# Kernel optimization log

Measured on AMD Instinct MI355X. Metric: run time of the kernel, lower is better.

Reference implementation:

```python
import jax, jax.numpy as jnp
import numpy as np
from jax import lax

B, PH, PW, D = 4, 256, 256, 128
WS, SS, NG, NH = 8, 4, 2, 4
HID = int(D * 2.0)
DC = D // 2  # ngram-context channel dim


def _window_partition(x, ws):
    b, h, w, c = x.shape
    x = x.reshape(b, h // ws, ws, w // ws, ws, c).transpose(0, 1, 3, 2, 4, 5)
    return x.reshape(-1, ws, ws, c), (h // ws, w // ws)


def _window_unpartition(win, nwin):
    wh, ww = nwin
    _, s1, s2, c = win.shape
    x = win.reshape(-1, wh, ww, s1, s2, c).transpose(0, 1, 3, 2, 4, 5)
    return x.reshape(-1, wh * s1, ww * s2, c)


def _rel_pos_index(wh, ww):
    coords = np.stack(np.meshgrid(np.arange(wh), np.arange(ww), indexing='ij')).reshape(2, -1)
    rel = (coords[:, :, None] - coords[:, None, :]).transpose(1, 2, 0)
    rel[:, :, 0] += wh - 1
    rel[:, :, 1] += ww - 1
    rel[:, :, 0] *= 2 * ww - 1
    return rel.sum(-1)  # [N, N]

RPI_MAIN = jnp.asarray(_rel_pos_index(WS, WS))
RPI_NG = jnp.asarray(_rel_pos_index(NG, NG))


def _layernorm(x, g, b, eps=1e-5):
    mu = x.mean(-1, keepdims=True)
    var = ((x - mu) ** 2).mean(-1, keepdims=True)
    return (x - mu) * lax.rsqrt(var + eps) * g + b


def _mhsa(x, qkv_w, qkv_b, proj_w, proj_b, bias_table, rpi, nheads, mask=None):
    b_, n, c = x.shape
    hd = c // nheads
    qkv = (x @ qkv_w.T + qkv_b).reshape(b_, n, 3, nheads, hd).transpose(2, 0, 3, 1, 4)
    q, k, v = qkv[0] * (hd ** -0.5), qkv[1], qkv[2]
    attn = jnp.einsum('bhnd,bhmd->bhnm', q, k) + bias_table[rpi].transpose(2, 0, 1)[None]
    if mask is not None:
        nw = mask.shape[0]
        attn = (attn.reshape(b_ // nw, nw, nheads, n, n) + mask[None, :, None]).reshape(b_, nheads, n, n)
    attn = jax.nn.softmax(attn, axis=-1)
    out = jnp.einsum('bhnm,bhmd->bhnd', attn, v).transpose(0, 2, 1, 3).reshape(b_, n, c)
    return out @ proj_w.T + proj_b


def _make_mask(ph, pw):
    img = np.zeros((ph, pw), np.float32)
    cnt = 0
    for h in (slice(0, -WS), slice(-WS, -SS), slice(-SS, None)):
        for w in (slice(0, -WS), slice(-WS, -SS), slice(-SS, None)):
            img[h, w] = cnt
            cnt += 1
    mw, _ = _window_partition(jnp.asarray(img)[None, :, :, None], WS)
    mw = mw.reshape(-1, WS * WS)
    diff = mw[:, None, :] - mw[:, :, None]
    return jnp.where(diff != 0, -100.0, 0.0)  # [wh*ww, WS*WS, WS*WS]


def _seq_refl_pad(u, back):
    # sequential reflective window pad by ngram-1 on H and W (front if back else end)
    nh, nw = u.shape[2], u.shape[3]
    if back:
        ih = np.concatenate([np.arange(1, NG), np.arange(nh)])
        iw = np.concatenate([np.arange(1, NG), np.arange(nw)])
    else:
        ih = np.concatenate([np.arange(nh), np.arange(nh - NG, nh - 1)])
        iw = np.concatenate([np.arange(nw), np.arange(nw - NG, nw - 1)])
    return u[:, :, ih][:, :, :, iw]


def _sliding_attn(u, ng_qkv_w, ng_qkv_b, ng_proj_w, ng_proj_b, ng_bias, wh, ww):
    # u: [B, DC, wh+NG-1, ww+NG-1]  (padded unigram)
    hi = (np.arange(wh)[:, None] + np.arange(NG)[None, :]).reshape(-1)
    wi = (np.arange(ww)[:, None] + np.arange(NG)[None, :]).reshape(-1)
    slide = u[:, :, hi][:, :, :, wi].transpose(0, 2, 3, 1)  # [B, wh*NG, ww*NG, DC]
    win, nwin = _window_partition(slide, NG)
    win = win.reshape(-1, NG * NG, DC)
    ctx = _mhsa(win, ng_qkv_w, ng_qkv_b, ng_proj_w, ng_proj_b, ng_bias, RPI_NG, NH)
    ctx = _window_unpartition(ctx.reshape(-1, NG, NG, DC), nwin)  # [B, wh*NG, ww*NG, DC]
    ctx = ctx.transpose(0, 3, 1, 2)
    b = ctx.shape[0]
    return ctx.reshape(b, DC, wh, NG, ww, NG).mean(axis=(3, 5))  # AvgPool2d(NG) -> [B, DC, wh, ww]


def reference(x, uni_w, uni_b, ng_qkv_w, ng_qkv_b, ng_proj_w, ng_proj_b, ng_bias,
              merge_w, merge_b, qkv_w, qkv_b, proj_w, proj_b, bias_table,
              n1_g, n1_b, n2_g, n2_b, fc1_w, fc1_b, fc2_w, fc2_b, ph, pw):
    b = x.shape[0]
    xi = x.reshape(b, ph, pw, D)
    wh, ww = ph // WS, pw // WS
    # --- NGram context ---
    xc = xi.transpose(0, 3, 1, 2)  # NCHW
    uni = lax.conv_general_dilated(xc, uni_w, (WS, WS), 'VALID', feature_group_count=DC,
                                   dimension_numbers=('NCHW', 'OIHW', 'NCHW'))
    uni = uni + uni_b[None, :, None, None]  # [B, DC, wh, ww]
    ctx_f = _sliding_attn(_seq_refl_pad(uni, False), ng_qkv_w, ng_qkv_b, ng_proj_w, ng_proj_b, ng_bias, wh, ww)
    ctx_b = _sliding_attn(_seq_refl_pad(uni, True), ng_qkv_w, ng_qkv_b, ng_proj_w, ng_proj_b, ng_bias, wh, ww)
    ctx = jnp.concatenate([ctx_f, ctx_b], axis=1)  # [B, D, wh, ww]
    ctx = jnp.einsum('bchw,oc->bohw', ctx, merge_w) + merge_b[None, :, None, None]  # 1x1 merge conv
    ctx = ctx.transpose(0, 2, 3, 1)  # [B, wh, ww, D]
    # --- inject context into semi-partitioned windows ---
    windows = xi.reshape(b, wh, WS, ww, WS, D).transpose(0, 1, 3, 2, 4, 5)  # [B, wh, ww, WS, WS, D]
    windows = windows + ctx[:, :, :, None, None, :]
    xw = windows.transpose(0, 1, 3, 2, 4, 5).reshape(b, ph, pw, D)
    # --- cyclic shift + masked window attention ---
    xw = jnp.roll(xw, (-SS, -SS), axis=(1, 2))
    win, _ = _window_partition(xw, WS)
    win = win.reshape(-1, WS * WS, D)
    mask = _make_mask(ph, pw)
    aw = _mhsa(win, qkv_w, qkv_b, proj_w, proj_b, bias_table, RPI_MAIN, NH, mask=mask)
    shifted = _window_unpartition(aw.reshape(-1, WS, WS, D), (wh, ww))  # [B, ph, pw, D]
    rev = jnp.roll(shifted, (SS, SS), axis=(1, 2)).reshape(b, ph * pw, D)
    # --- residual + post-branch layernorm, then FFN ---
    x1 = x + _layernorm(rev, n1_g, n1_b)
    h = jax.nn.gelu(x1 @ fc1_w.T + fc1_b, approximate=False)
    ffn = h @ fc2_w.T + fc2_b
    return x1 + _layernorm(ffn, n2_g, n2_b)


def setup_inputs() -> dict:
    key = jax.random.key(0)
    ks = jax.random.split(key, 12)
    w = lambda k, shape: jax.random.normal(k, shape, jnp.float32) * 0.02
    return {
        'x': jax.random.normal(ks[0], (B, PH * PW, D), jnp.float32),
        'uni_w': w(ks[1], (DC, 2, WS, WS)),
        'uni_b': jnp.zeros((DC,), jnp.float32),
        'ng_qkv_w': w(ks[2], (3 * DC, DC)),
        'ng_qkv_b': jnp.zeros((3 * DC,), jnp.float32),
        'ng_proj_w': w(ks[3], (DC, DC)),
        'ng_proj_b': jnp.zeros((DC,), jnp.float32),
        'ng_bias': w(ks[4], ((2 * NG - 1) ** 2, NH)),
        'merge_w': w(ks[5], (D, D)),
        'merge_b': jnp.zeros((D,), jnp.float32),
        'qkv_w': w(ks[6], (3 * D, D)),
        'qkv_b': jnp.zeros((3 * D,), jnp.float32),
        'proj_w': w(ks[7], (D, D)),
        'proj_b': jnp.zeros((D,), jnp.float32),
        'bias_table': w(ks[8], ((2 * WS - 1) ** 2, NH)),
        'n1_g': jnp.ones((D,), jnp.float32),
        'n1_b': jnp.zeros((D,), jnp.float32),
        'n2_g': jnp.ones((D,), jnp.float32),
        'n2_b': jnp.zeros((D,), jnp.float32),
        'fc1_w': w(ks[9], (HID, D)),
        'fc1_b': jnp.zeros((HID,), jnp.float32),
        'fc2_w': w(ks[10], (D, HID)),
        'fc2_b': jnp.zeros((D,), jnp.float32),
        'ph': PH,
        'pw': PW,
    }
```

## Files before the change

kernel.cpp:

```cpp
#include <hip/hip_runtime.h>

typedef __bf16 bf16x8 __attribute__((ext_vector_type(8)));
typedef float  f32x4  __attribute__((ext_vector_type(4)));

#define QSCALE 0.17677669529663687f
#define XF_LD 130

__device__ __forceinline__ f32x4 mfma16(bf16x8 a, bf16x8 b, f32x4 c) {
  return __builtin_amdgcn_mfma_f32_16x16x32_bf16(a, b, c, 0, 0, 0);
}

__device__ __forceinline__ int swz_idx(int row, int col, int rowChunks) {
  return row * (rowChunks << 3) + ((((col >> 3) ^ (row & 7)) << 3) | (col & 7));
}

__device__ __forceinline__ bf16x8 ld_tile(const __bf16* t, int rowChunks,
                                          int rowBase, int chunkBase, int lane) {
  int row = rowBase + (lane & 15);
  int c = (chunkBase + (lane >> 4)) ^ (row & 7);
  return *(const bf16x8*)(t + row * (rowChunks << 3) + (c << 3));
}

__device__ __forceinline__ bf16x8 ld_pack(const __bf16* pk, int nt, int ks,
                                          int ksteps, int lane) {
  int idx = ((nt * ksteps + ks) * 64 + lane) * 8;
  return *(const bf16x8*)(pk + idx);
}

__global__ void k_prep(const float* __restrict__ qkvw, const float* __restrict__ projw,
                       const float* __restrict__ fc1w, const float* __restrict__ fc2w,
                       const float* __restrict__ ngprojw, const float* __restrict__ ngprojb,
                       const float* __restrict__ mergew, const float* __restrict__ mergeb,
                       const float* __restrict__ bt,
                       const float* __restrict__ x, const float* __restrict__ uw,
                       const float* __restrict__ ub,
                       __bf16* __restrict__ pk, float* __restrict__ w12T,
                       float* __restrict__ fb, float* __restrict__ btf,
                       float* __restrict__ uni) {
  int blk = blockIdx.x;
  if (blk < 2048) {
    int bidx = blk * 2 + (threadIdx.x >> 7);
    int b = bidx >> 10, oh = (bidx >> 5) & 31, ow = bidx & 31;
    int d = threadIdx.x & 127;
    const float* xb = x + (((size_t)((b << 16) + ((oh << 3) << 8) + (ow << 3))) << 7) + d;
    const float* w = uw + d * 64;
    float acc = 0.f;
#pragma unroll
    for (int kh = 0; kh < 8; ++kh)
#pragma unroll
      for (int kw = 0; kw < 8; ++kw)
        acc += xb[(size_t)(((kh << 8) + kw)) << 7] * w[kh * 8 + kw];
    acc += __shfl_xor(acc, 1);
    if (!(d & 1)) uni[((size_t)bidx << 6) + (d >> 1)] = acc + ub[d >> 1];
  } else if (blk < 2560) {
    int i = (blk - 2048) * 256 + threadIdx.x;
    const float* src; int K; int e; int scaleQ = 0;
    if (i < 32768)      { src = qkvw;             K = 128; e = i;          scaleQ = 1; }
    else if (i < 49152) { src = qkvw + 256 * 128; K = 128; e = i - 32768; }
    else if (i < 65536) { src = projw;            K = 128; e = i - 49152; }
    else if (i < 98304) { src = fc1w;             K = 128; e = i - 65536; }
    else                { src = fc2w;             K = 256; e = i - 98304; }
    int i8 = e & 7, ln = (e >> 3) & 63, t = e >> 9;
    int ls = (K == 256) ? 3 : 2;
    int ks = t & ((1 << ls) - 1), nt = t >> ls;
    int row = (nt << 4) + (ln & 15);
    int k = (ks << 5) + ((ln >> 4) << 3) + i8;
    float v = src[row * K + k];
    if (scaleQ && row < 128) v *= QSCALE;
    pk[i] = (__bf16)v;
  } else if (blk < 2816) {
    int idx = (blk - 2560) * 256 + threadIdx.x;
    int v = idx >> 14, h = (idx >> 12) & 3, n = (idx >> 6) & 63, m = idx & 63;
    int s1n = n >> 3, s2n = n & 7, s1m = m >> 3, s2m = m & 7;
    int rpi = (s1n - s1m + 7) * 15 + (s2n - s2m + 7);
    float val = bt[rpi * 4 + h];
    if (((v & 1) && ((s1n < 4) != (s1m < 4))) ||
        ((v & 2) && ((s2n < 4) != (s2m < 4))))
      val -= 100.f;
    btf[idx] = val;
  } else {
    int idx = (blk - 2816) * 256 + threadIdx.x;
    if (idx < 16384) {
      int which = idx >> 13;
      int r = idx & 8191;
      int e = r >> 7, o = r & 127;
      float a = 0.f;
#pragma unroll 8
      for (int d = 0; d < 64; ++d)
        a += mergew[o * 128 + which * 64 + d] * ngprojw[d * 64 + e];
      w12T[idx] = a;
    } else if (idx < 16384 + 128) {
      int o = idx - 16384;
      float a = mergeb[o];
#pragma unroll 8
      for (int d = 0; d < 64; ++d)
        a += (mergew[o * 128 + d] + mergew[o * 128 + 64 + d]) * ngprojb[d];
      fb[o] = a;
    }
  }
}

__global__ void __launch_bounds__(256, 1)
k_ngram(const float* __restrict__ uni, const float* __restrict__ ngqkvw,
        const float* __restrict__ ngqkvb, const float* __restrict__ ngbias,
        const float* __restrict__ w12T, const float* __restrict__ fbg,
        float* __restrict__ ctx) {
  extern __shared__ float sm[];
  float* qkvT = sm;
  float* w1T  = qkvT + 12288;
  float* w2T  = w1T + 8192;
  float* tokl = w2T + 8192;
  float* qs   = tokl + 2304;
  float* prs  = qs + 6912;
  float* avgl = prs + 256;
  float* ngb  = avgl + 1024;
  float* fbs  = ngb + 192;
  float* nbias= fbs + 128;

  const int t = threadIdx.x;
  const int bidx = blockIdx.x;
  const int b = bidx >> 7, ii = (bidx >> 2) & 31, jq = bidx & 3;
  const int j0 = jq * 8;

#pragma unroll
  for (int it = 0; it < 12; ++it) {
    int f = it * 256 + t;
    int o = f >> 4, c4 = (f & 15) << 2;
    float4 v = *(const float4*)(ngqkvw + o * 64 + c4);
    float s = (o < 64) ? 0.25f : 1.f;
    qkvT[(c4 + 0) * 192 + o] = v.x * s;
    qkvT[(c4 + 1) * 192 + o] = v.y * s;
    qkvT[(c4 + 2) * 192 + o] = v.z * s;
    qkvT[(c4 + 3) * 192 + o] = v.w * s;
  }
#pragma unroll
  for (int it = 0; it < 16; ++it) {
    int f = (it * 256 + t) << 2;
    *(float4*)(w1T + f) = *(const float4*)(w12T + f);
  }
  if (t < 192) ngb[t] = ngqkvb[t] * (t < 64 ? 0.25f : 1.f);
  if (t < 128) fbs[t] = fbg[t];
  if (t < 36)  nbias[t] = ngbias[t];
  {
    int w = t >> 6, lane = t & 63;
    int dir = w >> 1, rr = w & 1;
    int pi = ii + rr;
    int srcr = (dir == 0) ? ((pi < 32) ? pi : 30) : ((pi == 0) ? 1 : pi - 1);
#pragma unroll
    for (int cc = 0; cc < 9; ++cc) {
      int pj = j0 + cc;
      int srcc = (dir == 0) ? ((pj < 32) ? pj : 30) : ((pj == 0) ? 1 : pj - 1);
      tokl[((dir * 2 + rr) * 9 + cc) * 64 + lane] =
          uni[(size_t)((b * 32 + srcr) * 32 + srcc) * 64 + lane];
    }
  }
  __syncthreads();

  {
    int w = t >> 6, lane = t & 63;
    for (int itp = 0; itp < 9; ++itp) {
      int pos = itp * 4 + w;
      const float* tk = tokl + pos * 64;
      float a0 = ngb[lane], a1 = ngb[64 + lane], a2 = ngb[128 + lane];
#pragma unroll 4
      for (int c = 0; c < 64; ++c) {
        float tv = tk[c];
        const float* qr = qkvT + c * 192;
        a0 += qr[lane] * tv;
        a1 += qr[64 + lane] * tv;
        a2 += qr[128 + lane] * tv;
      }
      float* dst = qs + pos * 192;
      dst[lane] = a0; dst[64 + lane] = a1; dst[128 + lane] = a2;
    }
  }
  __syncthreads();

  {
    int dw = t >> 4;
    int idx = t & 15, h = idx >> 2, p = idx & 3;
    int dir = dw >> 3, jl = dw & 7;
    const float* qp = qs + ((dir * 2 + (p >> 1)) * 9 + jl + (p & 1)) * 192 + h * 16;
    float s[4];
#pragma unroll
    for (int m = 0; m < 4; ++m) {
      const float* km = qs + ((dir * 2 + (m >> 1)) * 9 + jl + (m & 1)) * 192 + 64 + h * 16;
      float a = 0.f;
#pragma unroll
      for (int e = 0; e < 16; ++e) a += qp[e] * km[e];
      int bi2 = ((p >> 1) - (m >> 1) + 1) * 3 + ((p & 1) - (m & 1) + 1);
      s[m] = a + nbias[bi2 * 4 + h];
    }
    float mx = fmaxf(fmaxf(s[0], s[1]), fmaxf(s[2], s[3]));
    float e0 = __expf(s[0] - mx), e1 = __expf(s[1] - mx);
    float e2 = __expf(s[2] - mx), e3 = __expf(s[3] - mx);
    float inv = 1.f / (e0 + e1 + e2 + e3);
    float p0 = e0 * inv, p1 = e1 * inv, p2 = e2 * inv, p3 = e3 * inv;
    p0 += __shfl_xor(p0, 1); p0 += __shfl_xor(p0, 2);
    p1 += __shfl_xor(p1, 1); p1 += __shfl_xor(p1, 2);
    p2 += __shfl_xor(p2, 1); p2 += __shfl_xor(p2, 2);
    p3 += __shfl_xor(p3, 1); p3 += __shfl_xor(p3, 2);
    if (p == 0) {
      float* d = prs + (dw * 4 + h) * 4;
      d[0] = p0; d[1] = p1; d[2] = p2; d[3] = p3;
    }
  }
  __syncthreads();

  {
    int w = t >> 6, lane = t & 63;
#pragma unroll
    for (int it = 0; it < 4; ++it) {
      int dw = it * 4 + w;
      int dir = dw >> 3, jl = dw & 7;
      int h = lane >> 4;
      float a = 0.f;
#pragma unroll
      for (int m = 0; m < 4; ++m) {
        float pm = prs[(dw * 4 + h) * 4 + m];
        float vv = qs[((dir * 2 + (m >> 1)) * 9 + jl + (m & 1)) * 192 + 128 + lane];
        a += pm * vv;
      }
      avgl[dw * 64 + lane] = a * 0.25f;
    }
  }
  __syncthreads();

  {
#pragma unroll
    for (int it = 0; it < 4; ++it) {
      int id = it * 256 + t;
      int win = id >> 7, o = id & 127;
      const float* af = avgl + win * 64;
      const float* ab = avgl + (8 + win) * 64;
      float a = fbs[o];
#pragma unroll 4
      for (int c = 0; c < 64; ++c)
        a += w1T[c * 128 + o] * af[c] + w2T[c * 128 + o] * ab[c];
      int j = j0 + win;
      ctx[((size_t)((b * 32 + ii) * 32 + j)) * 128 + o] = a;
    }
  }
}

__global__ void __launch_bounds__(1024, 2)
k_main(const float* __restrict__ xin, const float* __restrict__ ctx,
       const __bf16* __restrict__ pk_qkv, const __bf16* __restrict__ pk_wv,
       const __bf16* __restrict__ pk_proj, const __bf16* __restrict__ pk_fc1,
       const __bf16* __restrict__ pk_fc2,
       const float* __restrict__ qkvb, const float* __restrict__ projb,
       const float* __restrict__ btf,
       const float* __restrict__ n1g, const float* __restrict__ n1b,
       const float* __restrict__ n2g, const float* __restrict__ n2b,
       const float* __restrict__ fc1b, const float* __restrict__ fc2b,
       float* __restrict__ outp) {
  extern __shared__ char smem[];
  __bf16* Xbf = (__bf16*)smem;
  __bf16* QO  = (__bf16*)(smem + 16 * 1024);
  __bf16* Kl  = (__bf16*)(smem + 32 * 1024);
  __bf16* Vt  = (__bf16*)(smem + 48 * 1024);
  __bf16* Pl  = (__bf16*)(smem + 64 * 1024);
  float*  Rf  = (float*)(smem + 48 * 1024);
  __bf16* Hl  = (__bf16*)(smem + 16 * 1024);
  float*  Ff  = (float*)(smem + 48 * 1024);

  const int widx = blockIdx.x;
  const int b = widx >> 10, wi = (widx >> 5) & 31, wj = widx & 31;
  const int tid = threadIdx.x;
  const int lane = tid & 63, wv = tid >> 6;
  const int lm = lane & 15, lg = lane >> 4;

  float xr[8];

  {
    int n = tid >> 4, c = tid & 15;
    int ts1 = n >> 3, ts2 = n & 7;
    int hh = ((wi << 3) + ts1 + 4) & 255;
    int ww = ((wj << 3) + ts2 + 4) & 255;
    const float* xs = xin + (((size_t)((b << 16) + (hh << 8) + ww)) << 7) + (c << 3);
    const float* cs = ctx + (((size_t)((((b << 5) + (hh >> 3)) << 5) + (ww >> 3))) << 7) + (c << 3);
    float4 xa = *(const float4*)xs;
    float4 xb = *(const float4*)(xs + 4);
    float4 ca = *(const float4*)cs;
    float4 cb = *(const float4*)(cs + 4);
    float v[8];
    v[0] = xa.x + ca.x; v[1] = xa.y + ca.y; v[2] = xa.z + ca.z; v[3] = xa.w + ca.w;
    v[4] = xb.x + cb.x; v[5] = xb.y + cb.y; v[6] = xb.z + cb.z; v[7] = xb.w + cb.w;
    bf16x8 p8;
#pragma unroll
    for (int e = 0; e < 8; ++e) p8[e] = (__bf16)v[e];
    *(bf16x8*)(Xbf + (n << 7) + ((c ^ (n & 7)) << 3)) = p8;
  }
  __syncthreads();

  {
    int ntG = wv;
    int col = (ntG << 4) + lm;
    float bias = (col < 128) ? qkvb[col] * QSCALE : qkvb[col];
    __bf16* dst = (col < 128) ? QO : Kl;
    int cc = col & 127;
    for (int mt = 0; mt < 4; ++mt) {
      bf16x8 af[4];
#pragma unroll
      for (int ks = 0; ks < 4; ++ks) af[ks] = ld_tile(Xbf, 16, mt * 16, ks * 4, lane);
      f32x4 acc = {0.f, 0.f, 0.f, 0.f};
#pragma unroll
      for (int ks = 0; ks < 4; ++ks)
        acc = mfma16(af[ks], ld_pack(pk_qkv, ntG, ks, 4, lane), acc);
#pragma unroll
      for (int r = 0; r < 4; ++r) {
        int row = mt * 16 + lg * 4 + r;
        dst[swz_idx(row, cc, 16)] = (__bf16)(acc[r] + bias);
      }
    }
  }
  {
    int mtG = wv >> 1;
    bf16x8 af[4];
#pragma unroll
    for (int ks = 0; ks < 4; ++ks) af[ks] = ld_pack(pk_wv, mtG, ks, 4, lane);
#pragma unroll
    for (int nt2 = 0; nt2 < 2; ++nt2) {
      int nt = ((wv & 1) << 1) + nt2;
      f32x4 acc = {0.f, 0.f, 0.f, 0.f};
#pragma unroll
      for (int ks = 0; ks < 4; ++ks)
        acc = mfma16(af[ks], ld_tile(Xbf, 16, nt * 16, ks * 4, lane), acc);
      int tok = (nt << 4) + lm;
#pragma unroll
      for (int r = 0; r < 4; ++r) {
        int ch = (mtG << 4) + lg * 4 + r;
        Vt[swz_idx(ch, tok, 8)] = (__bf16)(acc[r] + qkvb[256 + ch]);
      }
    }
  }
  __syncthreads();

  float rinv[4];
  const int h = wv >> 2, mq = wv & 3;
  __bf16* Pme = Pl + (h << 12);
  {
    bf16x8 aq = ld_tile(QO, 16, mq * 16, h * 4, lane);
    bf16x8 bk[4];
#pragma unroll
    for (int nt = 0; nt < 4; ++nt)
      bk[nt] = ld_tile(Kl, 16, nt * 16, h * 4, lane);
    f32x4 sc[4];
#pragma unroll
    for (int nt = 0; nt < 4; ++nt) {
      f32x4 z = {0.f, 0.f, 0.f, 0.f};
      sc[nt] = mfma16(aq, bk[nt], z);
    }
    const int variant = (wi == 31 ? 1 : 0) | (wj == 31 ? 2 : 0);
    const float* btw = btf + (((variant << 2) + h) << 12);
#pragma unroll
    for (int r = 0; r < 4; ++r) {
      int n = mq * 16 + lg * 4 + r;
      const float* brow = btw + (n << 6) + lm;
      float v[4];
#pragma unroll
      for (int nt = 0; nt < 4; ++nt)
        v[nt] = sc[nt][r] + brow[nt << 4];
      float mx = fmaxf(fmaxf(v[0], v[1]), fmaxf(v[2], v[3]));
#pragma unroll
      for (int d = 1; d < 16; d <<= 1) mx = fmaxf(mx, __shfl_xor(mx, d));
      float ssum = 0.f;
#pragma unroll
      for (int nt = 0; nt < 4; ++nt) { v[nt] = __expf(v[nt] - mx); ssum += v[nt]; }
#pragma unroll
      for (int d = 1; d < 16; d <<= 1) ssum += __shfl_xor(ssum, d);
      rinv[r] = 1.f / ssum;
#pragma unroll
      for (int nt = 0; nt < 4; ++nt)
        Pme[swz_idx(n, nt * 16 + lm, 8)] = (__bf16)v[nt];
    }
  }

  {
    bf16x8 ap[2], bv[2][2];
#pragma unroll
    for (int nt = 0; nt < 2; ++nt)
#pragma unroll
      for (int ks = 0; ks < 2; ++ks)
        bv[nt][ks] = ld_tile(Vt, 8, h * 32 + nt * 16, ks * 4, lane);
#pragma unroll
    for (int ks = 0; ks < 2; ++ks)
      ap[ks] = ld_tile(Pme, 8, mq * 16, ks * 4, lane);
#pragma unroll
    for (int nt = 0; nt < 2; ++nt) {
      f32x4 acc = {0.f, 0.f, 0.f, 0.f};
      acc = mfma16(ap[0], bv[nt][0], acc);
      acc = mfma16(ap[1], bv[nt][1], acc);
      int cc = h * 32 + nt * 16 + lm;
#pragma unroll
      for (int r = 0; r < 4; ++r) {
        int row = mq * 16 + lg * 4 + r;
        QO[swz_idx(row, cc, 16)] = (__bf16)(acc[r] * rinv[r]);
      }
    }
  }
  __syncthreads();

  {
    int ntG = wv >> 1;
    int col = (ntG << 4) + lm;
    float pb = projb[col];
#pragma unroll
    for (int mt2 = 0; mt2 < 2; ++mt2) {
      int mt = ((wv & 1) << 1) + mt2;
      bf16x8 ao[4];
#pragma unroll
      for (int ks = 0; ks < 4; ++ks) ao[ks] = ld_tile(QO, 16, mt * 16, ks * 4, lane);
      f32x4 acc = {0.f, 0.f, 0.f, 0.f};
#pragma unroll
      for (int ks = 0; ks < 4; ++ks)
        acc = mfma16(ao[ks], ld_pack(pk_proj, ntG, ks, 4, lane), acc);
#pragma unroll
      for (int r = 0; r < 4; ++r) {
        int row = mt * 16 + lg * 4 + r;
        Rf[row * XF_LD + col] = acc[r] + pb;
      }
    }
  }
  __syncthreads();

  {
    int n = tid >> 4, c = tid & 15;
    int ts1 = n >> 3, ts2 = n & 7;
    int hh = ((wi << 3) + ts1 + 4) & 255;
    int ww = ((wj << 3) + ts2 + 4) & 255;
    const float* xp = xin + (((size_t)((b << 16) + (hh << 8) + ww)) << 7) + (c << 3);
    float xv[8];
    {
      float4 v4 = *(const float4*)xp;
      float4 w4 = *(const float4*)(xp + 4);
      xv[0] = v4.x; xv[1] = v4.y; xv[2] = v4.z; xv[3] = v4.w;
      xv[4] = w4.x; xv[5] = w4.y; xv[6] = w4.z; xv[7] = w4.w;
    }
    const float* rrow = Rf + n * XF_LD + (c << 3);
    float vals[8];
    float sum1 = 0.f, sum2 = 0.f;
#pragma unroll
    for (int jj = 0; jj < 8; ++jj) { float v = rrow[jj]; vals[jj] = v; sum1 += v; sum2 += v * v; }
    sum1 += __shfl_xor(sum1, 1); sum1 += __shfl_xor(sum1, 2);
    sum1 += __shfl_xor(sum1, 4); sum1 += __shfl_xor(sum1, 8);
    sum2 += __shfl_xor(sum2, 1); sum2 += __shfl_xor(sum2, 2);
    sum2 += __shfl_xor(sum2, 4); sum2 += __shfl_xor(sum2, 8);
    float mean = sum1 * 0.0078125f;
    float var = sum2 * 0.0078125f - mean * mean;
    float rstd = rsqrtf(var + 1e-5f);
    bf16x8 p8;
#pragma unroll
    for (int e = 0; e < 8; ++e) {
      int d = (c << 3) + e;
      float ln = (vals[e] - mean) * rstd * n1g[d] + n1b[d];
      float x1 = xv[e] + ln;
      xr[e] = x1;
      p8[e] = (__bf16)x1;
    }
    *(bf16x8*)(Xbf + (n << 7) + ((c ^ (n & 7)) << 3)) = p8;
  }
  __syncthreads();

  {
    int ntG = wv;
    int col = (ntG << 4) + lm;
    float b1 = fc1b[col];
    for (int mt = 0; mt < 4; ++mt) {
      bf16x8 a1[4];
#pragma unroll
      for (int ks = 0; ks < 4; ++ks) a1[ks] = ld_tile(Xbf, 16, mt * 16, ks * 4, lane);
      f32x4 acc = {0.f, 0.f, 0.f, 0.f};
#pragma unroll
      for (int ks = 0; ks < 4; ++ks)
        acc = mfma16(a1[ks], ld_pack(pk_fc1, ntG, ks, 4, lane), acc);
#pragma unroll
      for (int r = 0; r < 4; ++r) {
        int row = mt * 16 + lg * 4 + r;
        float hv = acc[r] + b1;
        float u = hv * (0.7978845608f + 0.0356774081f * hv * hv);
        float e = __expf(2.f * u);
        hv = hv - hv / (e + 1.f);
        Hl[swz_idx(row, col, 32)] = (__bf16)hv;
      }
    }
  }
  __syncthreads();

  {
    int ntG = wv >> 1;
    int col = (ntG << 4) + lm;
    float b2 = fc2b[col];
#pragma unroll
    for (int mt2 = 0; mt2 < 2; ++mt2) {
      int mt = ((wv & 1) << 1) + mt2;
      bf16x8 a2[8];
#pragma unroll
      for (int ks = 0; ks < 8; ++ks) a2[ks] = ld_tile(Hl, 32, mt * 16, ks * 4, lane);
      f32x4 acc = {0.f, 0.f, 0.f, 0.f};
#pragma unroll
      for (int ks = 0; ks < 8; ++ks)
        acc = mfma16(a2[ks], ld_pack(pk_fc2, ntG, ks, 8, lane), acc);
#pragma unroll
      for (int r = 0; r < 4; ++r) {
        int row = mt * 16 + lg * 4 + r;
        Ff[row * XF_LD + col] = acc[r] + b2;
      }
    }
  }
  __syncthreads();

  {
    int n = tid >> 4, c = tid & 15;
    const float* frow = Ff + n * XF_LD + (c << 3);
    float vals[8];
    float sum1 = 0.f, sum2 = 0.f;
#pragma unroll
    for (int jj = 0; jj < 8; ++jj) { float v = frow[jj]; vals[jj] = v; sum1 += v; sum2 += v * v; }
    sum1 += __shfl_xor(sum1, 1); sum1 += __shfl_xor(sum1, 2);
    sum1 += __shfl_xor(sum1, 4); sum1 += __shfl_xor(sum1, 8);
    sum2 += __shfl_xor(sum2, 1); sum2 += __shfl_xor(sum2, 2);
    sum2 += __shfl_xor(sum2, 4); sum2 += __shfl_xor(sum2, 8);
    float mean = sum1 * 0.0078125f;
    float var = sum2 * 0.0078125f - mean * mean;
    float rstd = rsqrtf(var + 1e-5f);
    int ts1 = n >> 3, ts2 = n & 7;
    int hh = ((wi << 3) + ts1 + 4) & 255;
    int ww = ((wj << 3) + ts2 + 4) & 255;
    float* op = outp + (((size_t)((b << 16) + (hh << 8) + ww)) << 7) + (c << 3);
    int dbase = (c << 3);
    float4 o4a, o4b;
    o4a.x = xr[0] + (vals[0] - mean) * rstd * n2g[dbase + 0] + n2b[dbase + 0];
    o4a.y = xr[1] + (vals[1] - mean) * rstd * n2g[dbase + 1] + n2b[dbase + 1];
    o4a.z = xr[2] + (vals[2] - mean) * rstd * n2g[dbase + 2] + n2b[dbase + 2];
    o4a.w = xr[3] + (vals[3] - mean) * rstd * n2g[dbase + 3] + n2b[dbase + 3];
    o4b.x = xr[4] + (vals[4] - mean) * rstd * n2g[dbase + 4] + n2b[dbase + 4];
    o4b.y = xr[5] + (vals[5] - mean) * rstd * n2g[dbase + 5] + n2b[dbase + 5];
    o4b.z = xr[6] + (vals[6] - mean) * rstd * n2g[dbase + 6] + n2b[dbase + 6];
    o4b.w = xr[7] + (vals[7] - mean) * rstd * n2g[dbase + 7] + n2b[dbase + 7];
    *(float4*)op = o4a;
    *(float4*)(op + 4) = o4b;
  }
}

extern "C" void kernel_launch(void* const* d_in, const int* in_sizes, int n_in,
                              void* d_out, int out_size, void* d_ws, size_t ws_size,
                              hipStream_t stream) {
  const float* x      = (const float*)d_in[0];
  const float* uni_w  = (const float*)d_in[1];
  const float* uni_b  = (const float*)d_in[2];
  const float* ngqkvw = (const float*)d_in[3];
  const float* ngqkvb = (const float*)d_in[4];
  const float* ngprojw= (const float*)d_in[5];
  const float* ngprojb= (const float*)d_in[6];
  const float* ngbias = (const float*)d_in[7];
  const float* mergew = (const float*)d_in[8];
  const float* mergeb = (const float*)d_in[9];
  const float* qkvw   = (const float*)d_in[10];
  const float* qkvb   = (const float*)d_in[11];
  const float* projw  = (const float*)d_in[12];
  const float* projb  = (const float*)d_in[13];
  const float* bt     = (const float*)d_in[14];
  const float* n1g    = (const float*)d_in[15];
  const float* n1b    = (const float*)d_in[16];
  const float* n2g    = (const float*)d_in[17];
  const float* n2b    = (const float*)d_in[18];
  const float* fc1w   = (const float*)d_in[19];
  const float* fc1b   = (const float*)d_in[20];
  const float* fc2w   = (const float*)d_in[21];
  const float* fc2b   = (const float*)d_in[22];

  char* ws = (char*)d_ws;
  float*  uni = (float*)ws;
  float*  ctx = (float*)(ws + (1 << 20));
  __bf16* pk  = (__bf16*)(ws + (3 << 20));
  __bf16* pk_qkv  = pk;
  __bf16* pk_wv   = pk + 32768;
  __bf16* pk_proj = pk + 49152;
  __bf16* pk_fc1  = pk + 65536;
  __bf16* pk_fc2  = pk + 98304;
  float*  w12T = (float*)(ws + (7 << 19));
  float*  fb   = w12T + 16384;
  float*  btf  = (float*)(ws + 3840 * 1024);

  k_prep<<<2881, 256, 0, stream>>>(qkvw, projw, fc1w, fc2w, ngprojw, ngprojb,
                                   mergew, mergeb, bt, x, uni_w, uni_b,
                                   pk, w12T, fb, btf, uni);
  k_ngram<<<512, 256, 158096, stream>>>(uni, ngqkvw, ngqkvb, ngbias, w12T, fb, ctx);
  k_main<<<4096, 1024, 98304, stream>>>(x, ctx, pk_qkv, pk_wv, pk_proj, pk_fc1, pk_fc2,
                                        qkvb, projb, btf, n1g, n1b, n2g, n2b, fc1b, fc2b,
                                        (float*)d_out);
}
```

Baseline: 332.4 us.

## Swap MFMA operand order so accumulators hold channels, enabling vectorized LDS stores

Every GEMM in the fused window-attention block (QKV, scores, PV, proj, fc1, fc2) now passes weights as the A operand and activations as B. Each lane's four accumulator values then cover four consecutive channels of one token, so results are written to LDS as bf16x4 or float4 vectors instead of four scalar stores. Weight fragments are hoisted out of the token loops, and the bias table is transposed to match. Softmax is now reduced per query column with two cross-half shuffles, and normalization is folded into P before the PV matmul. The float row stride is padded to 132 so the float4 stores stay aligned. Rounding changes slightly because P is normalized before conversion to bf16.

```diff
diff --git a/kernel.cpp b/kernel.cpp
--- a/kernel.cpp
+++ b/kernel.cpp
@@ -1,10 +1,11 @@
 #include <hip/hip_runtime.h>
 
 typedef __bf16 bf16x8 __attribute__((ext_vector_type(8)));
+typedef __bf16 bf16x4 __attribute__((ext_vector_type(4)));
 typedef float  f32x4  __attribute__((ext_vector_type(4)));
 
 #define QSCALE 0.17677669529663687f
-#define XF_LD 130
+#define XF_LD 132
 
 __device__ __forceinline__ f32x4 mfma16(bf16x8 a, bf16x8 b, f32x4 c) {
   return __builtin_amdgcn_mfma_f32_16x16x32_bf16(a, b, c, 0, 0, 0);
@@ -70,8 +71,8 @@
     pk[i] = (__bf16)v;
   } else if (blk < 2816) {
     int idx = (blk - 2560) * 256 + threadIdx.x;
-    int v = idx >> 14, h = (idx >> 12) & 3, n = (idx >> 6) & 63, m = idx & 63;
-    int s1n = n >> 3, s2n = n & 7, s1m = m >> 3, s2m = m & 7;
+    int v = idx >> 14, h = (idx >> 12) & 3, kk = (idx >> 6) & 63, q = idx & 63;
+    int s1n = q >> 3, s2n = q & 7, s1m = kk >> 3, s2m = kk & 7;
     int rpi = (s1n - s1m + 7) * 15 + (s2n - s2m + 7);
     float val = bt[rpi * 4 + h];
     if (((v & 1) && ((s1n < 4) != (s1m < 4))) ||
@@ -295,23 +296,28 @@
 
   {
     int ntG = wv;
-    int col = (ntG << 4) + lm;
-    float bias = (col < 128) ? qkvb[col] * QSCALE : qkvb[col];
-    __bf16* dst = (col < 128) ? QO : Kl;
-    int cc = col & 127;
-    for (int mt = 0; mt < 4; ++mt) {
-      bf16x8 af[4];
-#pragma unroll
-      for (int ks = 0; ks < 4; ++ks) af[ks] = ld_tile(Xbf, 16, mt * 16, ks * 4, lane);
+    bf16x8 wf[4];
+#pragma unroll
+    for (int ks = 0; ks < 4; ++ks) wf[ks] = ld_pack(pk_qkv, ntG, ks, 4, lane);
+    int col0 = (ntG << 4) + (lg << 2);
+    float bias[4];
+#pragma unroll
+    for (int r = 0; r < 4; ++r)
+      bias[r] = (ntG < 8) ? qkvb[col0 + r] * QSCALE : qkvb[col0 + r];
+    __bf16* dst = (ntG < 8) ? QO : Kl;
+    int cc0 = col0 & 127;
+    for (int nt = 0; nt < 4; ++nt) {
+      bf16x8 xf[4];
+#pragma unroll
+      for (int ks = 0; ks < 4; ++ks) xf[ks] = ld_tile(Xbf, 16, nt * 16, ks * 4, lane);
       f32x4 acc = {0.f, 0.f, 0.f, 0.f};
 #pragma unroll
-      for (int ks = 0; ks < 4; ++ks)
-        acc = mfma16(af[ks], ld_pack(pk_qkv, ntG, ks, 4, lane), acc);
-#pragma unroll
-      for (int r = 0; r < 4; ++r) {
-        int row = mt * 16 + lg * 4 + r;
-        dst[swz_idx(row, cc, 16)] = (__bf16)(acc[r] + bias);
-      }
+      for (int ks = 0; ks < 4; ++ks) acc = mfma16(wf[ks], xf[ks], acc);
+      int tok = nt * 16 + lm;
+      bf16x4 p4;
+#pragma unroll
+      for (int r = 0; r < 4; ++r) p4[r] = (__bf16)(acc[r] + bias[r]);
+      *(bf16x4*)(dst + (tok << 7) + ((((cc0 >> 3) ^ (tok & 7)) << 3) | (cc0 & 7))) = p4;
     }
   }
   {
@@ -336,7 +342,6 @@
   }
   __syncthreads();
 
-  float rinv[4];
   const int h = wv >> 2, mq = wv & 3;
   __bf16* Pme = Pl + (h << 12);
   {
@@ -349,77 +354,85 @@
 #pragma unroll
     for (int nt = 0; nt < 4; ++nt) {
       f32x4 z = {0.f, 0.f, 0.f, 0.f};
-      sc[nt] = mfma16(aq, bk[nt], z);
+      sc[nt] = mfma16(bk[nt], aq, z);
     }
     const int variant = (wi == 31 ? 1 : 0) | (wj == 31 ? 2 : 0);
     const float* btw = btf + (((variant << 2) + h) << 12);
-#pragma unroll
-    for (int r = 0; r < 4; ++r) {
-      int n = mq * 16 + lg * 4 + r;
-      const float* brow = btw + (n << 6) + lm;
-      float v[4];
-#pragma unroll
-      for (int nt = 0; nt < 4; ++nt)
-        v[nt] = sc[nt][r] + brow[nt << 4];
-      float mx = fmaxf(fmaxf(v[0], v[1]), fmaxf(v[2], v[3]));
-#pragma unroll
-      for (int d = 1; d < 16; d <<= 1) mx = fmaxf(mx, __shfl_xor(mx, d));
-      float ssum = 0.f;
-#pragma unroll
-      for (int nt = 0; nt < 4; ++nt) { v[nt] = __expf(v[nt] - mx); ssum += v[nt]; }
-#pragma unroll
-      for (int d = 1; d < 16; d <<= 1) ssum += __shfl_xor(ssum, d);
-      rinv[r] = 1.f / ssum;
-#pragma unroll
-      for (int nt = 0; nt < 4; ++nt)
-        Pme[swz_idx(n, nt * 16 + lm, 8)] = (__bf16)v[nt];
-    }
-  }
-
-  {
-    bf16x8 ap[2], bv[2][2];
-#pragma unroll
-    for (int nt = 0; nt < 2; ++nt)
-#pragma unroll
-      for (int ks = 0; ks < 2; ++ks)
-        bv[nt][ks] = ld_tile(Vt, 8, h * 32 + nt * 16, ks * 4, lane);
+    const int q = mq * 16 + lm;
+    float v[4][4];
+    float mx = -1e30f;
+#pragma unroll
+    for (int nt = 0; nt < 4; ++nt)
+#pragma unroll
+      for (int r = 0; r < 4; ++r) {
+        int kk = nt * 16 + (lg << 2) + r;
+        float s = sc[nt][r] + btw[(kk << 6) + q];
+        v[nt][r] = s;
+        mx = fmaxf(mx, s);
+      }
+    mx = fmaxf(mx, __shfl_xor(mx, 16));
+    mx = fmaxf(mx, __shfl_xor(mx, 32));
+    float ssum = 0.f;
+#pragma unroll
+    for (int nt = 0; nt < 4; ++nt)
+#pragma unroll
+      for (int r = 0; r < 4; ++r) { v[nt][r] = __expf(v[nt][r] - mx); ssum += v[nt][r]; }
+    ssum += __shfl_xor(ssum, 16);
+    ssum += __shfl_xor(ssum, 32);
+    float rinv = 1.f / ssum;
+#pragma unroll
+    for (int nt = 0; nt < 4; ++nt) {
+      bf16x4 p4;
+#pragma unroll
+      for (int r = 0; r < 4; ++r) p4[r] = (__bf16)(v[nt][r] * rinv);
+      int k0 = nt * 16 + (lg << 2);
+      *(bf16x4*)(Pme + (q << 6) + ((((k0 >> 3) ^ (q & 7)) << 3) | (k0 & 7))) = p4;
+    }
+  }
+
+  {
+    bf16x8 ap[2];
 #pragma unroll
     for (int ks = 0; ks < 2; ++ks)
       ap[ks] = ld_tile(Pme, 8, mq * 16, ks * 4, lane);
 #pragma unroll
     for (int nt = 0; nt < 2; ++nt) {
+      bf16x8 bv0 = ld_tile(Vt, 8, h * 32 + nt * 16, 0, lane);
+      bf16x8 bv1 = ld_tile(Vt, 8, h * 32 + nt * 16, 4, lane);
       f32x4 acc = {0.f, 0.f, 0.f, 0.f};
-      acc = mfma16(ap[0], bv[nt][0], acc);
-      acc = mfma16(ap[1], bv[nt][1], acc);
-      int cc = h * 32 + nt * 16 + lm;
-#pragma unroll
-      for (int r = 0; r < 4; ++r) {
-        int row = mq * 16 + lg * 4 + r;
-        QO[swz_idx(row, cc, 16)] = (__bf16)(acc[r] * rinv[r]);
-      }
+      acc = mfma16(bv0, ap[0], acc);
+      acc = mfma16(bv1, ap[1], acc);
+      int q = mq * 16 + lm;
+      int ch0 = h * 32 + nt * 16 + (lg << 2);
+      bf16x4 p4;
+#pragma unroll
+      for (int r = 0; r < 4; ++r) p4[r] = (__bf16)acc[r];
+      *(bf16x4*)(QO + (q << 7) + ((((ch0 >> 3) ^ (q & 7)) << 3) | (ch0 & 7))) = p4;
     }
   }
   __syncthreads();
 
   {
     int ntG = wv >> 1;
-    int col = (ntG << 4) + lm;
-    float pb = projb[col];
+    int ch0 = (ntG << 4) + (lg << 2);
+    float pb[4];
+#pragma unroll
+    for (int r = 0; r < 4; ++r) pb[r] = projb[ch0 + r];
+    bf16x8 wf[4];
+#pragma unroll
+    for (int ks = 0; ks < 4; ++ks) wf[ks] = ld_pack(pk_proj, ntG, ks, 4, lane);
 #pragma unroll
     for (int mt2 = 0; mt2 < 2; ++mt2) {
       int mt = ((wv & 1) << 1) + mt2;
-      bf16x8 ao[4];
-#pragma unroll
-      for (int ks = 0; ks < 4; ++ks) ao[ks] = ld_tile(QO, 16, mt * 16, ks * 4, lane);
       f32x4 acc = {0.f, 0.f, 0.f, 0.f};
 #pragma unroll
       for (int ks = 0; ks < 4; ++ks)
-        acc = mfma16(ao[ks], ld_pack(pk_proj, ntG, ks, 4, lane), acc);
-#pragma unroll
-      for (int r = 0; r < 4; ++r) {
-        int row = mt * 16 + lg * 4 + r;
-        Rf[row * XF_LD + col] = acc[r] + pb;
-      }
+        acc = mfma16(wf[ks], ld_tile(QO, 16, mt * 16, ks * 4, lane), acc);
+      int tok = mt * 16 + lm;
+      float4 st;
+      st.x = acc[0] + pb[0]; st.y = acc[1] + pb[1];
+      st.z = acc[2] + pb[2]; st.w = acc[3] + pb[3];
+      *(float4*)(Rf + tok * XF_LD + ch0) = st;
     }
   }
   __syncthreads();
@@ -464,48 +477,54 @@
 
   {
     int ntG = wv;
-    int col = (ntG << 4) + lm;
-    float b1 = fc1b[col];
-    for (int mt = 0; mt < 4; ++mt) {
-      bf16x8 a1[4];
-#pragma unroll
-      for (int ks = 0; ks < 4; ++ks) a1[ks] = ld_tile(Xbf, 16, mt * 16, ks * 4, lane);
+    int ch0 = (ntG << 4) + (lg << 2);
+    float b1[4];
+#pragma unroll
+    for (int r = 0; r < 4; ++r) b1[r] = fc1b[ch0 + r];
+    bf16x8 wf[4];
+#pragma unroll
+    for (int ks = 0; ks < 4; ++ks) wf[ks] = ld_pack(pk_fc1, ntG, ks, 4, lane);
+    for (int nt = 0; nt < 4; ++nt) {
       f32x4 acc = {0.f, 0.f, 0.f, 0.f};
 #pragma unroll
       for (int ks = 0; ks < 4; ++ks)
-        acc = mfma16(a1[ks], ld_pack(pk_fc1, ntG, ks, 4, lane), acc);
+        acc = mfma16(wf[ks], ld_tile(Xbf, 16, nt * 16, ks * 4, lane), acc);
+      int tok = nt * 16 + lm;
+      bf16x4 p4;
 #pragma unroll
       for (int r = 0; r < 4; ++r) {
-        int row = mt * 16 + lg * 4 + r;
-        float hv = acc[r] + b1;
+        float hv = acc[r] + b1[r];
         float u = hv * (0.7978845608f + 0.0356774081f * hv * hv);
         float e = __expf(2.f * u);
         hv = hv - hv / (e + 1.f);
-        Hl[swz_idx(row, col, 32)] = (__bf16)hv;
+        p4[r] = (__bf16)hv;
       }
+      *(bf16x4*)(Hl + (tok << 8) + ((((ch0 >> 3) ^ (tok & 7)) << 3) | (ch0 & 7))) = p4;
     }
   }
   __syncthreads();
 
   {
     int ntG = wv >> 1;
-    int col = (ntG << 4) + lm;
-    float b2 = fc2b[col];
+    int ch0 = (ntG << 4) + (lg << 2);
+    float b2[4];
+#pragma unroll
+    for (int r = 0; r < 4; ++r) b2[r] = fc2b[ch0 + r];
+    bf16x8 wf[8];
+#pragma unroll
+    for (int ks = 0; ks < 8; ++ks) wf[ks] = ld_pack(pk_fc2, ntG, ks, 8, lane);
 #pragma unroll
     for (int mt2 = 0; mt2 < 2; ++mt2) {
       int mt = ((wv & 1) << 1) + mt2;
-      bf16x8 a2[8];
-#pragma unroll
-      for (int ks = 0; ks < 8; ++ks) a2[ks] = ld_tile(Hl, 32, mt * 16, ks * 4, lane);
       f32x4 acc = {0.f, 0.f, 0.f, 0.f};
 #pragma unroll
       for (int ks = 0; ks < 8; ++ks)
-        acc = mfma16(a2[ks], ld_pack(pk_fc2, ntG, ks, 8, lane), acc);
-#pragma unroll
-      for (int r = 0; r < 4; ++r) {
-        int row = mt * 16 + lg * 4 + r;
-        Ff[row * XF_LD + col] = acc[r] + b2;
-      }
+        acc = mfma16(wf[ks], ld_tile(Hl, 32, mt * 16, ks * 4, lane), acc);
+      int tok = mt * 16 + lm;
+      float4 st;
+      st.x = acc[0] + b2[0]; st.y = acc[1] + b2[1];
+      st.z = acc[2] + b2[2]; st.w = acc[3] + b2[3];
+      *(float4*)(Ff + tok * XF_LD + ch0) = st;
     }
   }
   __syncthreads();
```

Measured after the change: 303.7 us. 8.7% less time.
